# Kernel optimization log

Hardware: AMD Instinct MI355X
Metric: run time of the kernel (lower is better)

The kernel has to match this reference:

```python
import jax, jax.numpy as jnp
import numpy as np

TEMPERATURE = 0.07


def setup_inputs() -> dict:
    key = jax.random.key(0)
    embeddings = jax.random.normal(key, (16384, 256), dtype=jnp.float32)
    return {"embeddings": embeddings}


def reference(embeddings) -> jnp.ndarray:
    # L2 normalize rows (torch F.normalize uses eps clamp 1e-12)
    norm = jnp.maximum(jnp.linalg.norm(embeddings, axis=1, keepdims=True), 1e-12)
    emb = embeddings / norm
    # [N, N] similarity, temperature-scaled logits
    logits = jnp.matmul(emb, emb.T) / TEMPERATURE
    # cross entropy against diagonal labels (labels[i] = i)
    logp = jax.nn.log_softmax(logits, axis=1)
    loss = -jnp.mean(jnp.diagonal(logp))
    return loss
```

## Files before the change

kernel.cpp:

```cpp
#include <hip/hip_runtime.h>
#include <hip/hip_bf16.h>

typedef __bf16 bf16;
typedef __attribute__((ext_vector_type(8))) __bf16 bf16x8;
typedef __attribute__((ext_vector_type(4))) __bf16 bf16x4;
typedef __attribute__((ext_vector_type(16))) float f32x16;

#define N_ROWS 16384
#define DIM 256
#define NJC 512
#define NBLKS 768
#define TPB 43
#define NTILES 33024
#define SQK1 4.53981608f
#define LN2F 0.69314718056f

#define WS_T_OFF (N_ROWS * DIM * 2)
#define WS_D_OFF (WS_T_OFF + N_ROWS * 4)

#define GLOAD_LDS(g, l)                                        \
    __builtin_amdgcn_global_load_lds(                          \
        (const __attribute__((address_space(1))) void*)(g),    \
        (__attribute__((address_space(3))) void*)(l), 16, 0, 0)

__global__ void __launch_bounds__(256) normalize_kernel(const float* __restrict__ in,
                                                        bf16* __restrict__ out,
                                                        float* __restrict__ Tg,
                                                        float* __restrict__ Dg,
                                                        float* __restrict__ loss_out) {
    if (blockIdx.x == 0 && threadIdx.x == 0) loss_out[0] = 0.0f;
    if (blockIdx.x < 64) Tg[blockIdx.x * 256 + threadIdx.x] = 0.0f;

    const int row  = blockIdx.x * 4 + (threadIdx.x >> 6);
    const int lane = threadIdx.x & 63;
    const float4* rp = (const float4*)(in + (size_t)row * DIM);
    float4 v = rp[lane];
    float ss = v.x * v.x + v.y * v.y + v.z * v.z + v.w * v.w;
#pragma unroll
    for (int m = 1; m < 64; m <<= 1) ss += __shfl_xor(ss, m, 64);
    float inv = SQK1 / fmaxf(sqrtf(ss), 1e-12f);
    bf16x4 o;
    o[0] = (bf16)(v.x * inv);
    o[1] = (bf16)(v.y * inv);
    o[2] = (bf16)(v.z * inv);
    o[3] = (bf16)(v.w * inv);
    *(bf16x4*)(out + (size_t)row * DIM + lane * 4) = o;

    float f0 = (float)o[0], f1 = (float)o[1], f2 = (float)o[2], f3 = (float)o[3];
    float s2 = f0 * f0 + f1 * f1 + f2 * f2 + f3 * f3;
#pragma unroll
    for (int m = 1; m < 64; m <<= 1) s2 += __shfl_xor(s2, m, 64);
    if (lane == 0) Dg[row] = s2;
}

#define TREE16(R, out)                                                     \
    do {                                                                   \
        float w8[8], w4[4], w2[2], w1, g_;                                 \
        _Pragma("unroll") for (int i_ = 0; i_ < 8; ++i_) {                 \
            g_ = (lo & 16) ? R[i_] : R[i_ + 8];                            \
            w8[i_] = ((lo & 16) ? R[i_ + 8] : R[i_]) + __shfl_xor(g_, 16); \
        }                                                                  \
        _Pragma("unroll") for (int i_ = 0; i_ < 4; ++i_) {                 \
            g_ = (lo & 8) ? w8[i_] : w8[i_ + 4];                           \
            w4[i_] = ((lo & 8) ? w8[i_ + 4] : w8[i_]) + __shfl_xor(g_, 8); \
        }                                                                  \
        _Pragma("unroll") for (int i_ = 0; i_ < 2; ++i_) {                 \
            g_ = (lo & 4) ? w4[i_] : w4[i_ + 2];                           \
            w2[i_] = ((lo & 4) ? w4[i_ + 2] : w4[i_]) + __shfl_xor(g_, 4); \
        }                                                                  \
        g_ = (lo & 2) ? w2[0] : w2[1];                                     \
        w1 = ((lo & 2) ? w2[1] : w2[0]) + __shfl_xor(g_, 2);               \
        out = w1 + __shfl_xor(w1, 1);                                      \
    } while (0)

__global__ void __launch_bounds__(256, 3)
loss_kernel(const bf16* __restrict__ A, float* __restrict__ Tg) {
    __shared__ bf16 Bs[3][32 * DIM];

    const int tid = threadIdx.x;
    const int w  = tid >> 6;
    const int l  = tid & 63;
    const int lo = l & 31, hi = l >> 5;

    const int bid = (int)(blockIdx.x & 7) * (NBLKS / 8) + (int)(blockIdx.x >> 3);
    const int tbeg = bid * TPB;

    int it = 0;
    while (2 * (it + 1) * (257 - (it + 1)) <= tbeg) ++it;
    int jc = 4 * it + (tbeg - 2 * it * (257 - it));

#define ADV(ITX, JCX)                                                        \
    do { if (++JCX == NJC) { ++ITX; JCX = 4 * ITX; } } while (0)
    int it1 = it, jc1 = jc; ADV(it1, jc1);
    int it2 = it1, jc2 = jc1; ADV(it2, jc2);

    bf16x8 af[16];
#define LOAD_AF(ITX)                                                         \
    do {                                                                     \
        const bf16* ap_ = A + (size_t)((ITX) * 128 + w * 32 + lo) * DIM + hi * 8; \
        _Pragma("unroll") for (int k_ = 0; k_ < 16; ++k_)                    \
            af[k_] = *(const bf16x8*)(ap_ + k_ * 16);                        \
    } while (0)
    LOAD_AF(it);

    float s0[16];
#pragma unroll
    for (int r = 0; r < 16; ++r) s0[r] = 0.f;

    const int s_dma = l & 31;
    const int rl    = l >> 5;
    int vo[4];
#pragma unroll
    for (int q = 0; q < 4; ++q) {
        const int c = (s_dma & 24) | ((s_dma & 7) ^ ((q * 2 + rl) & 7));
        vo[q] = rl * DIM + c * 8;
    }

    const int rbase = lo * DIM;
    const int mx7 = lo & 7;

#define ISSUE(jcn_, BUF)                                                     \
    do {                                                                     \
        const bf16* tb_ = A + (size_t)((jcn_) * 32 + w * 8) * DIM;           \
        bf16* lb_ = (BUF) + (w * 8) * DIM;                                   \
        _Pragma("unroll") for (int q_ = 0; q_ < 4; ++q_) {                   \
            GLOAD_LDS(tb_ + (q_ * 2) * DIM + vo[q_],                         \
                      lb_ + (q_ * 2) * DIM);                                 \
        }                                                                    \
    } while (0)

#define FLUSH_ROWS                                                           \
    do {                                                                     \
        float tr_;                                                           \
        TREE16(s0, tr_);                                                     \
        const int r_ = (lo >> 1) & 15;                                       \
        const int rowoff_ = (r_ & 3) + 8 * (r_ >> 2) + 4 * hi;               \
        if ((l & 1) == 0)                                                    \
            atomicAdd(&Tg[it * 128 + w * 32 + rowoff_], tr_);                \
    } while (0)

    int t = 0;

#define BODY(BR, BW, WN0, WL)                                                \
    do {                                                                     \
        if (t + 2 < TPB) {                                                   \
            asm volatile("s_waitcnt vmcnt(" #WN0 ")" ::: "memory");          \
        } else {                                                             \
            asm volatile("s_waitcnt vmcnt(" #WL ")" ::: "memory");           \
        }                                                                    \
        asm volatile("s_barrier" ::: "memory");                              \
        if (t + 2 < TPB) ISSUE(jc2, BW);                                     \
        f32x16 c0;                                                           \
        _Pragma("unroll") for (int r_ = 0; r_ < 16; ++r_) c0[r_] = 0.f;      \
        __builtin_amdgcn_s_setprio(1);                                       \
        _Pragma("unroll") for (int k_ = 0; k_ < 16; ++k_) {                  \
            const int cc_ = k_ * 2 + hi;                                     \
            const int slot_ = (cc_ & 24) | ((cc_ & 7) ^ mx7);                \
            bf16x8 b_ = *(const bf16x8*)&(BR)[rbase + slot_ * 8];            \
            c0 = __builtin_amdgcn_mfma_f32_32x32x16_bf16(af[k_], b_, c0, 0, 0, 0); \
        }                                                                    \
        __builtin_amdgcn_s_setprio(0);                                       \
        float cs_ = 0.f;                                                     \
        _Pragma("unroll") for (int r_ = 0; r_ < 16; ++r_) {                  \
            float e_ = __builtin_amdgcn_exp2f(c0[r_]);                       \
            s0[r_] += e_;                                                    \
            cs_ += e_;                                                       \
        }                                                                    \
        cs_ += __shfl_xor(cs_, 32);                                          \
         \
         \
        const float fv_ = ((jc >> 2) == it) ? 0.0f : cs_;                    \
        if (hi == 0) atomicAdd(&Tg[jc * 32 + lo], fv_);                      \
        if (t + 1 < TPB) {                                                   \
            if (it1 != it) {                                                 \
                FLUSH_ROWS;                                                  \
                LOAD_AF(it1);                                                \
                _Pragma("unroll") for (int r_ = 0; r_ < 16; ++r_) s0[r_] = 0.f; \
            }                                                                \
            it = it1; jc = jc1; it1 = it2; jc1 = jc2; ADV(it2, jc2);         \
        }                                                                    \
        ++t;                                                                 \
    } while (0)

    ISSUE(jc, &Bs[0][0]);
    ISSUE(jc1, &Bs[1][0]);

    BODY(&Bs[0][0], &Bs[2][0], 4, 0);
    while (t < TPB) {
        BODY(&Bs[1][0], &Bs[0][0], 5, 1);
        if (t >= TPB) break;
        BODY(&Bs[2][0], &Bs[1][0], 5, 1);
        if (t >= TPB) break;
        BODY(&Bs[0][0], &Bs[2][0], 5, 1);
    }
    FLUSH_ROWS;

#undef ISSUE
#undef BODY
#undef ADV
#undef FLUSH_ROWS
#undef LOAD_AF
}

__global__ void __launch_bounds__(256) final_kernel(const float* __restrict__ Tg,
                                                    const float* __restrict__ Dg,
                                                    float* __restrict__ out) {
    __shared__ float red[4];
    const int i = blockIdx.x * 256 + threadIdx.x;
    float c = LN2F * (__log2f(Tg[i]) - Dg[i]) * (1.0f / (float)N_ROWS);
#pragma unroll
    for (int m = 1; m < 64; m <<= 1) c += __shfl_xor(c, m, 64);
    if ((threadIdx.x & 63) == 0) red[threadIdx.x >> 6] = c;
    __syncthreads();
    if (threadIdx.x == 0)
        atomicAdd(out, red[0] + red[1] + red[2] + red[3]);
}

extern "C" void kernel_launch(void* const* d_in, const int* in_sizes, int n_in,
                              void* d_out, int out_size, void* d_ws, size_t ws_size,
                              hipStream_t stream) {
    const float* emb = (const float*)d_in[0];
    float* out = (float*)d_out;
    bf16* Abf = (bf16*)d_ws;
    float* Tg = (float*)((char*)d_ws + WS_T_OFF);
    float* Dg = (float*)((char*)d_ws + WS_D_OFF);

    hipLaunchKernelGGL(normalize_kernel, dim3(N_ROWS / 4), dim3(256), 0, stream,
                       emb, Abf, Tg, Dg, out);
    hipLaunchKernelGGL(loss_kernel, dim3(NBLKS), dim3(256), 0, stream,
                       Abf, Tg);
    hipLaunchKernelGGL(final_kernel, dim3(N_ROWS / 256), dim3(256), 0, stream,
                       Tg, Dg, out);
}
```

Before: 148.5 us.

## Store normalized embeddings in MFMA fragment layout and load B directly from global

The normalize kernel now writes bf16 rows in a tiled layout matching the MFMA operand fragment, so each lane's 16-byte load is contiguous. The loss kernel drops the triple-buffered LDS pipeline (global_load_lds, waitcnts, swizzle) and reads B fragments straight from global/L2. It also removes the XCD-aware block remapping and the priority hints. This cuts LDS traffic and bookkeeping, but exposes global load latency to the MFMA loop with no explicit prefetch, and all four waves now read the same B tile separately.

```diff
diff --git a/kernel.cpp b/kernel.cpp
--- a/kernel.cpp
+++ b/kernel.cpp
@@ -5,6 +5,7 @@
 typedef __attribute__((ext_vector_type(8))) __bf16 bf16x8;
 typedef __attribute__((ext_vector_type(4))) __bf16 bf16x4;
 typedef __attribute__((ext_vector_type(16))) float f32x16;
+typedef unsigned long long u64;
 
 #define N_ROWS 16384
 #define DIM 256
@@ -12,16 +13,12 @@
 #define NBLKS 768
 #define TPB 43
 #define NTILES 33024
+#define TILE_ELEMS 8192
 #define SQK1 4.53981608f
 #define LN2F 0.69314718056f
 
 #define WS_T_OFF (N_ROWS * DIM * 2)
 #define WS_D_OFF (WS_T_OFF + N_ROWS * 4)
-
-#define GLOAD_LDS(g, l)                                        \
-    __builtin_amdgcn_global_load_lds(                          \
-        (const __attribute__((address_space(1))) void*)(g),    \
-        (__attribute__((address_space(3))) void*)(l), 16, 0, 0)
 
 __global__ void __launch_bounds__(256) normalize_kernel(const float* __restrict__ in,
                                                         bf16* __restrict__ out,
@@ -44,7 +41,17 @@
     o[1] = (bf16)(v.y * inv);
     o[2] = (bf16)(v.z * inv);
     o[3] = (bf16)(v.w * inv);
-    *(bf16x4*)(out + (size_t)row * DIM + lane * 4) = o;
+
+    {
+        const int tile = row >> 5, lo = row & 31;
+        const int k  = lane >> 2;
+        const int hi = (lane >> 1) & 1;
+        const int h  = lane & 1;
+        union { bf16x4 v4; u64 u; } pun;
+        pun.v4 = o;
+        *(u64*)(out + (size_t)tile * TILE_ELEMS + k * 512 + (hi * 32 + lo) * 8 + h * 4)
+            = pun.u;
+    }
 
     float f0 = (float)o[0], f1 = (float)o[1], f2 = (float)o[2], f3 = (float)o[3];
     float s2 = f0 * f0 + f1 * f1 + f2 * f2 + f3 * f3;
@@ -74,32 +81,25 @@
     } while (0)
 
 __global__ void __launch_bounds__(256, 3)
-loss_kernel(const bf16* __restrict__ A, float* __restrict__ Tg) {
-    __shared__ bf16 Bs[3][32 * DIM];
-
+loss_kernel(const bf16* __restrict__ A2, float* __restrict__ Tg) {
     const int tid = threadIdx.x;
     const int w  = tid >> 6;
     const int l  = tid & 63;
     const int lo = l & 31, hi = l >> 5;
+    (void)hi;
 
-    const int bid = (int)(blockIdx.x & 7) * (NBLKS / 8) + (int)(blockIdx.x >> 3);
-    const int tbeg = bid * TPB;
+    const int tbeg = blockIdx.x * TPB;
 
     int it = 0;
     while (2 * (it + 1) * (257 - (it + 1)) <= tbeg) ++it;
     int jc = 4 * it + (tbeg - 2 * it * (257 - it));
 
-#define ADV(ITX, JCX)                                                        \
-    do { if (++JCX == NJC) { ++ITX; JCX = 4 * ITX; } } while (0)
-    int it1 = it, jc1 = jc; ADV(it1, jc1);
-    int it2 = it1, jc2 = jc1; ADV(it2, jc2);
-
     bf16x8 af[16];
 #define LOAD_AF(ITX)                                                         \
     do {                                                                     \
-        const bf16* ap_ = A + (size_t)((ITX) * 128 + w * 32 + lo) * DIM + hi * 8; \
+        const bf16* ap_ = A2 + (size_t)((ITX) * 4 + w) * TILE_ELEMS + l * 8; \
         _Pragma("unroll") for (int k_ = 0; k_ < 16; ++k_)                    \
-            af[k_] = *(const bf16x8*)(ap_ + k_ * 16);                        \
+            af[k_] = *(const bf16x8*)(ap_ + k_ * 512);                       \
     } while (0)
     LOAD_AF(it);
 
@@ -107,97 +107,53 @@
 #pragma unroll
     for (int r = 0; r < 16; ++r) s0[r] = 0.f;
 
-    const int s_dma = l & 31;
-    const int rl    = l >> 5;
-    int vo[4];
-#pragma unroll
-    for (int q = 0; q < 4; ++q) {
-        const int c = (s_dma & 24) | ((s_dma & 7) ^ ((q * 2 + rl) & 7));
-        vo[q] = rl * DIM + c * 8;
-    }
-
-    const int rbase = lo * DIM;
-    const int mx7 = lo & 7;
-
-#define ISSUE(jcn_, BUF)                                                     \
-    do {                                                                     \
-        const bf16* tb_ = A + (size_t)((jcn_) * 32 + w * 8) * DIM;           \
-        bf16* lb_ = (BUF) + (w * 8) * DIM;                                   \
-        _Pragma("unroll") for (int q_ = 0; q_ < 4; ++q_) {                   \
-            GLOAD_LDS(tb_ + (q_ * 2) * DIM + vo[q_],                         \
-                      lb_ + (q_ * 2) * DIM);                                 \
-        }                                                                    \
-    } while (0)
-
 #define FLUSH_ROWS                                                           \
     do {                                                                     \
         float tr_;                                                           \
         TREE16(s0, tr_);                                                     \
         const int r_ = (lo >> 1) & 15;                                       \
-        const int rowoff_ = (r_ & 3) + 8 * (r_ >> 2) + 4 * hi;               \
+        const int rowoff_ = (r_ & 3) + 8 * (r_ >> 2) + 4 * (l >> 5);         \
         if ((l & 1) == 0)                                                    \
             atomicAdd(&Tg[it * 128 + w * 32 + rowoff_], tr_);                \
     } while (0)
 
-    int t = 0;
+    for (int t = 0; t < TPB; ++t) {
+        asm volatile("s_barrier" ::: "memory");
 
-#define BODY(BR, BW, WN0, WL)                                                \
-    do {                                                                     \
-        if (t + 2 < TPB) {                                                   \
-            asm volatile("s_waitcnt vmcnt(" #WN0 ")" ::: "memory");          \
-        } else {                                                             \
-            asm volatile("s_waitcnt vmcnt(" #WL ")" ::: "memory");           \
-        }                                                                    \
-        asm volatile("s_barrier" ::: "memory");                              \
-        if (t + 2 < TPB) ISSUE(jc2, BW);                                     \
-        f32x16 c0;                                                           \
-        _Pragma("unroll") for (int r_ = 0; r_ < 16; ++r_) c0[r_] = 0.f;      \
-        __builtin_amdgcn_s_setprio(1);                                       \
-        _Pragma("unroll") for (int k_ = 0; k_ < 16; ++k_) {                  \
-            const int cc_ = k_ * 2 + hi;                                     \
-            const int slot_ = (cc_ & 24) | ((cc_ & 7) ^ mx7);                \
-            bf16x8 b_ = *(const bf16x8*)&(BR)[rbase + slot_ * 8];            \
-            c0 = __builtin_amdgcn_mfma_f32_32x32x16_bf16(af[k_], b_, c0, 0, 0, 0); \
-        }                                                                    \
-        __builtin_amdgcn_s_setprio(0);                                       \
-        float cs_ = 0.f;                                                     \
-        _Pragma("unroll") for (int r_ = 0; r_ < 16; ++r_) {                  \
-            float e_ = __builtin_amdgcn_exp2f(c0[r_]);                       \
-            s0[r_] += e_;                                                    \
-            cs_ += e_;                                                       \
-        }                                                                    \
-        cs_ += __shfl_xor(cs_, 32);                                          \
-         \
-         \
-        const float fv_ = ((jc >> 2) == it) ? 0.0f : cs_;                    \
-        if (hi == 0) atomicAdd(&Tg[jc * 32 + lo], fv_);                      \
-        if (t + 1 < TPB) {                                                   \
-            if (it1 != it) {                                                 \
-                FLUSH_ROWS;                                                  \
-                LOAD_AF(it1);                                                \
-                _Pragma("unroll") for (int r_ = 0; r_ < 16; ++r_) s0[r_] = 0.f; \
-            }                                                                \
-            it = it1; jc = jc1; it1 = it2; jc1 = jc2; ADV(it2, jc2);         \
-        }                                                                    \
-        ++t;                                                                 \
-    } while (0)
+        const bf16* tb = A2 + (size_t)jc * TILE_ELEMS + l * 8;
+        f32x16 c0;
+#pragma unroll
+        for (int r = 0; r < 16; ++r) c0[r] = 0.f;
+#pragma unroll
+        for (int k = 0; k < 16; ++k) {
+            bf16x8 b = *(const bf16x8*)(tb + k * 512);
+            c0 = __builtin_amdgcn_mfma_f32_32x32x16_bf16(af[k], b, c0, 0, 0, 0);
+        }
 
-    ISSUE(jc, &Bs[0][0]);
-    ISSUE(jc1, &Bs[1][0]);
+        float cs = 0.f;
+#pragma unroll
+        for (int r = 0; r < 16; ++r) {
+            float e = __builtin_amdgcn_exp2f(c0[r]);
+            s0[r] += e;
+            cs += e;
+        }
+        cs += __shfl_xor(cs, 32);
+        if (((jc >> 2) != it) && (l >> 5) == 0)
+            atomicAdd(&Tg[jc * 32 + lo], cs);
 
-    BODY(&Bs[0][0], &Bs[2][0], 4, 0);
-    while (t < TPB) {
-        BODY(&Bs[1][0], &Bs[0][0], 5, 1);
-        if (t >= TPB) break;
-        BODY(&Bs[2][0], &Bs[1][0], 5, 1);
-        if (t >= TPB) break;
-        BODY(&Bs[0][0], &Bs[2][0], 5, 1);
+        if (t + 1 < TPB) {
+            if (++jc == NJC) {
+                FLUSH_ROWS;
+                ++it;
+                jc = 4 * it;
+                LOAD_AF(it);
+#pragma unroll
+                for (int r = 0; r < 16; ++r) s0[r] = 0.f;
+            }
+        }
     }
     FLUSH_ROWS;
 
-#undef ISSUE
-#undef BODY
-#undef ADV
 #undef FLUSH_ROWS
 #undef LOAD_AF
 }
```

After: 177.1 us. 19.3% more time.
